# Performance work log

Measured on AMD Instinct MI355X. Metric: run time of the kernel, lower is better.

## Reference

```python
import jax, jax.numpy as jnp
import numpy as np

B, LX, LY = 64, 64, 64
E = 512          # enc_hid_size
D = 512          # dec_hid_size
NE = 512         # n_embed
H = 8            # n_head
E2 = 2 * E       # bidirectional annotation width


def setup_inputs() -> dict:
    key = jax.random.key(0)
    ks = iter(jax.random.split(key, 40))
    def rn(shape, scale=1.0):
        return jax.random.normal(next(ks), shape, dtype=jnp.float32) * scale
    s = lambda f: 1.0 / np.sqrt(f)
    return dict(
        xs_h=rn((B, LX, E2)),
        ys_e=rn((B, LY, NE)),
        xs_mask=jnp.ones((B, LX), jnp.float32),
        ys_mask=jnp.ones((B, LY), jnp.float32),
        W_sinit=rn((E2, D), s(E2)), b_sinit=jnp.zeros((D,), jnp.float32),
        W_keys=rn((E2, D), s(E2)),
        Wx_cell=rn((NE, 3 * D), s(NE)), bx_cell=jnp.zeros((3, D), jnp.float32), gx_cell=jnp.ones((3, D), jnp.float32),
        Wh_cell=rn((D, 3 * D), s(D)), gh_cell=jnp.ones((3, D), jnp.float32),
        Wx_cond=rn((E2, 3 * D), s(E2)), bx_cond=jnp.zeros((3, D), jnp.float32), gx_cond=jnp.ones((3, D), jnp.float32),
        Wh_cond=rn((D, 3 * D), s(D)), gh_cond=jnp.ones((3, D), jnp.float32),
        Wq=rn((D, D), s(D)), bq=jnp.zeros((D,), jnp.float32),
        V_att=rn((D, H), s(D)),
        Wo=rn((E2, E2), s(E2)), bo=jnp.zeros((E2,), jnp.float32),
        Wy=rn((NE, D), s(NE)), by=jnp.zeros((D,), jnp.float32),
        Wc=rn((E2, D), s(E2)), bc=jnp.zeros((D,), jnp.float32),
        Ws=rn((D, D), s(D)), bs=jnp.zeros((D,), jnp.float32),
    )


def _ln(v, eps=1e-5):
    mu = v.mean(-1, keepdims=True)
    var = ((v - mu) ** 2).mean(-1, keepdims=True)
    return (v - mu) * jax.lax.rsqrt(var + eps)


def _ln_gru(x, h, m, Wx, bx, gx, Wh, gh):
    # layer-normalized GRU transition cell (TransiLNCell), mask keeps old state on padding
    Bn = x.shape[0]
    ax = _ln((x @ Wx).reshape(Bn, 3, D)) * gx + bx   # (B,3,D), LN per gate chunk
    ah = _ln((h @ Wh).reshape(Bn, 3, D)) * gh
    r = jax.nn.sigmoid(ax[:, 0] + ah[:, 0])
    z = jax.nn.sigmoid(ax[:, 1] + ah[:, 1])
    hc = jnp.tanh(ax[:, 2] + r * ah[:, 2])
    hn = (1.0 - z) * h + z * hc
    return m[:, None] * hn + (1.0 - m[:, None]) * h


def _attend(s, xs_h, uh, xs_mask, Wq, bq, V, Wo, bo):
    # multihead additive attention: per-head additive scores, head-split values
    q = s @ Wq + bq                                   # (B,D)
    hid = jnp.tanh(uh + q[:, None, :])                # (B,L,D)
    e = jnp.einsum('bld,dh->blh', hid, V)             # (B,L,H)
    e = jnp.where(xs_mask[:, :, None] > 0, e, -1e9)
    alpha = jax.nn.softmax(e, axis=1)                 # (B,L,H)
    Bn, L, _ = xs_h.shape
    vals = xs_h.reshape(Bn, L, H, E2 // H)
    ctx = jnp.einsum('blh,blhv->bhv', alpha, vals).reshape(Bn, E2)
    return alpha, ctx @ Wo + bo


def reference(xs_h, ys_e, xs_mask, ys_mask,
              W_sinit, b_sinit, W_keys,
              Wx_cell, bx_cell, gx_cell, Wh_cell, gh_cell,
              Wx_cond, bx_cond, gx_cond, Wh_cond, gh_cond,
              Wq, bq, V_att, Wo, bo,
              Wy, by, Wc, bc, Ws, bs):
    # init_state: precompute attention keys, mean-pool annotations -> s0
    uh = xs_h @ W_keys                                          # (B,LX,D)
    pooled = (xs_h * xs_mask[:, :, None]).sum(1) / xs_mask.sum(1)[:, None]
    s0 = jnp.tanh(pooled @ W_sinit + b_sinit)                   # (B,D)

    def step(s_tm1, inp):
        y_tm1, ym = inp                                         # (B,NE), (B,)
        state = _ln_gru(y_tm1, s_tm1, ym, Wx_cell, bx_cell, gx_cell, Wh_cell, gh_cell)
        _, ctx = _attend(state, xs_h, uh, xs_mask, Wq, bq, V_att, Wo, bo)
        ctx = ctx * ym[:, None]
        s_t = _ln_gru(ctx, state, ym, Wx_cond, bx_cond, gx_cond, Wh_cond, gh_cond)
        # step_out: fused 3-way linear sum + tanh (max_out=False, dropout off in eval)
        logit = jnp.tanh(y_tm1 @ Wy + by + ctx @ Wc + bc + s_t @ Ws + bs)
        return s_t, logit

    ys_t = jnp.swapaxes(ys_e, 0, 1)      # (LY,B,NE) time-major
    ym_t = jnp.swapaxes(ys_mask, 0, 1)   # (LY,B)
    _, logits = jax.lax.scan(step, s0, (ys_t, ym_t))
    logits = jnp.swapaxes(logits, 0, 1)  # (B,LY,D)
    return logits * ys_mask[:, :, None]
```

## Files before the change

### kernel.cpp

```cpp
#include <hip/hip_runtime.h>
#include <math.h>

#define TPB 512
#define NWG 256

__device__ __forceinline__ float g_ld(const float* p){
    return __hip_atomic_load(p, __ATOMIC_RELAXED, __HIP_MEMORY_SCOPE_AGENT);
}
__device__ __forceinline__ void g_st(float* p, float v){
    __hip_atomic_store(p, v, __ATOMIC_RELAXED, __HIP_MEMORY_SCOPE_AGENT);
}
__device__ __forceinline__ float sigm(float x){ return 1.f/(1.f+expf(-x)); }

__global__ __launch_bounds__(TPB) void decoder_persistent(
    const float* __restrict__ xs_h, const float* __restrict__ ys_e,
    const float* __restrict__ xs_mask, const float* __restrict__ ys_mask,
    const float* __restrict__ W_sinit, const float* __restrict__ b_sinit,
    const float* __restrict__ W_keys,
    const float* __restrict__ Wx_cell, const float* __restrict__ bx_cell,
    const float* __restrict__ gx_cell, const float* __restrict__ Wh_cell,
    const float* __restrict__ gh_cell,
    const float* __restrict__ Wx_cond, const float* __restrict__ bx_cond,
    const float* __restrict__ gx_cond, const float* __restrict__ Wh_cond,
    const float* __restrict__ gh_cond,
    const float* __restrict__ Wq, const float* __restrict__ bq,
    const float* __restrict__ V_att, const float* __restrict__ Wo,
    const float* __restrict__ bo, const float* __restrict__ Wy,
    const float* __restrict__ by, const float* __restrict__ Wc,
    const float* __restrict__ bc, const float* __restrict__ Wsm,
    const float* __restrict__ bs,
    float* __restrict__ out, float* __restrict__ ws)
{
    const int w    = blockIdx.x;
    const int tid  = threadIdx.x;
    const int lane = tid & 63, wv = tid >> 6;
    const int i    = w & 7;
    const int grp  = w >> 3;
    const int b0   = grp * 2;

    unsigned* cntg = (unsigned*)ws + (size_t)grp * 16;
    float* AXn  = ws + 1024;
    float* uhP  = AXn  + (size_t)64*64*1536;
    float* YWbP = uhP  + (size_t)256*16*512;
    float* PB   = YWbP + (size_t)256*2*64*64;
    float* pb     = PB + (size_t)grp * 18432;
    float* tmpH_  = pb;
    float* tmpHC_ = pb + 3072;
    float* tmpXC_ = pb + 6144;
    float* qb_    = pb + 9216;
    float* e_     = pb + 10240;
    float* ctx0_  = pb + 11264;
    float* ctx_   = pb + 13312;
    float* pool_  = pb + 15360;
    float* s0_    = pb + 17408;

    __shared__ float sal[2][512];
    __shared__ float sbl[2][512];
    __shared__ float al[2][64];
    __shared__ float outcl[2][64];
    __shared__ float xml[2][64];
    __shared__ float red[8][24];
    __shared__ float red2[24];
    __shared__ float arena[13056];
    float* xv   = arena;
    float* comb = arena + 2048;

    unsigned gen = 0;
    auto gbar = [&](){
        __syncthreads();
        ++gen;
        if (tid == 0){
            __hip_atomic_fetch_add(cntg, 1u, __ATOMIC_RELAXED, __HIP_MEMORY_SCOPE_AGENT);
            while (__hip_atomic_load(cntg, __ATOMIC_RELAXED, __HIP_MEMORY_SCOPE_AGENT) < 8u*gen)
                __builtin_amdgcn_s_sleep(2);
        }
        asm volatile("" ::: "memory");
        __syncthreads();
    };

    auto breduce = [&](float* v, int nv){
        for (int n = 0; n < nv; ++n){
            float x = v[n];
            #pragma unroll
            for (int o = 32; o; o >>= 1) x += __shfl_xor(x, o);
            v[n] = x;
        }
        if (lane == 0) for (int n = 0; n < nv; ++n) red[wv][n] = v[n];
        __syncthreads();
        if (tid < nv){ float s = 0.f; for (int q = 0; q < 8; ++q) s += red[q][tid]; red2[tid] = s; }
        __syncthreads();
        for (int n = 0; n < nv; ++n) v[n] = red2[n];
    };

    auto gemv2 = [&](const float* Wa, int lda, int ca,
                     const float* Wb, int ldb, int cb, int CGA,
                     const float* x0, const float* x1, int K)->float{
        int cg = tid & 63, kq = tid >> 6;
        const float* W; int ld, col;
        if (cg < CGA){ W = Wa; ld = lda; col = ca + 4*cg; }
        else         { W = Wb; ld = ldb; col = cb + 4*(cg - CGA); }
        int Kq = K >> 3;
        const float* wp = W + (size_t)(kq*Kq)*ld + col;
        const float* xa = x0 + kq*Kq;
        const float* xb = x1 + kq*Kq;
        float a0=0,a1=0,a2=0,a3=0, c0=0,c1=0,c2=0,c3=0;
        for (int kk = 0; kk < Kq; kk += 8){
            float4 wr[8];
            #pragma unroll
            for (int u = 0; u < 8; ++u) wr[u] = *(const float4*)(wp + (size_t)(kk+u)*ld);
            #pragma unroll
            for (int u = 0; u < 8; ++u){
                float xA = xa[kk+u], xB = xb[kk+u];
                a0 = fmaf(xA, wr[u].x, a0); a1 = fmaf(xA, wr[u].y, a1);
                a2 = fmaf(xA, wr[u].z, a2); a3 = fmaf(xA, wr[u].w, a3);
                c0 = fmaf(xB, wr[u].x, c0); c1 = fmaf(xB, wr[u].y, c1);
                c2 = fmaf(xB, wr[u].z, c2); c3 = fmaf(xB, wr[u].w, c3);
            }
        }
        float* cp = comb + tid*9;
        cp[0]=a0; cp[1]=a1; cp[2]=a2; cp[3]=a3;
        cp[4]=c0; cp[5]=c1; cp[6]=c2; cp[7]=c3;
        __syncthreads();
        int bb = tid >> 8, c = tid & 255, cgq = c >> 2, j = c & 3;
        float s = 0.f;
        #pragma unroll
        for (int q = 0; q < 8; ++q) s += comb[(q*64 + cgq)*9 + bb*4 + j];
        __syncthreads();
        return s;
    };

    if (tid < 128) xml[tid>>6][tid&63] = xs_mask[(size_t)(b0 + (tid>>6))*64 + (tid&63)];
    __syncthreads();

    {
        int c4 = tid & 127, kq = tid >> 7;
        unsigned base[16];
        #pragma unroll
        for (int j = 0; j < 16; ++j){
            int bb = j >> 3, l = i*8 + (j & 7);
            base[j] = (unsigned)(((b0+bb)*64 + l)*1024 + kq*256);
        }
        const float* wp = W_keys + (size_t)(kq*256)*512 + 4*c4;
        float4 acc[16];
        #pragma unroll
        for (int j = 0; j < 16; ++j) acc[j] = make_float4(0.f,0.f,0.f,0.f);
        for (int kk = 0; kk < 256; ++kk){
            float4 wr = *(const float4*)(wp + (size_t)kk*512);
            #pragma unroll
            for (int j = 0; j < 16; ++j){
                float xr = xs_h[base[j] + kk];
                acc[j].x = fmaf(xr, wr.x, acc[j].x); acc[j].y = fmaf(xr, wr.y, acc[j].y);
                acc[j].z = fmaf(xr, wr.z, acc[j].z); acc[j].w = fmaf(xr, wr.w, acc[j].w);
            }
        }
        for (int r = 0; r < 16; ++r){
            float* cp = arena + tid*5;
            cp[0]=acc[r].x; cp[1]=acc[r].y; cp[2]=acc[r].z; cp[3]=acc[r].w;
            __syncthreads();
            int c = tid; float s = 0.f;
            #pragma unroll
            for (int q = 0; q < 4; ++q) s += arena[(q*128 + (c>>2))*5 + (c&3)];
            uhP[((size_t)w*16 + r)*512 + c] = s;
            __syncthreads();
        }
    }

    for (int g = 0; g < 3; ++g){
        int c4 = tid & 127, kq = tid >> 7;
        unsigned base[16];
        #pragma unroll
        for (int j = 0; j < 16; ++j){
            int bb = j >> 3, t = i*8 + (j & 7);
            base[j] = (unsigned)(((b0+bb)*64 + t)*512 + kq*128);
        }
        const float* wp = Wx_cell + (size_t)(kq*128)*1536 + g*512 + 4*c4;
        float4 acc[16];
        #pragma unroll
        for (int j = 0; j < 16; ++j) acc[j] = make_float4(0.f,0.f,0.f,0.f);
        for (int kk = 0; kk < 128; ++kk){
            float4 wr = *(const float4*)(wp + (size_t)kk*1536);
            #pragma unroll
            for (int j = 0; j < 16; ++j){
                float xr = ys_e[base[j] + kk];
                acc[j].x = fmaf(xr, wr.x, acc[j].x); acc[j].y = fmaf(xr, wr.y, acc[j].y);
                acc[j].z = fmaf(xr, wr.z, acc[j].z); acc[j].w = fmaf(xr, wr.w, acc[j].w);
            }
        }
        for (int r = 0; r < 16; ++r){
            float* cp = arena + tid*5;
            cp[0]=acc[r].x; cp[1]=acc[r].y; cp[2]=acc[r].z; cp[3]=acc[r].w;
            __syncthreads();
            int c = tid; float val = 0.f;
            #pragma unroll
            for (int q = 0; q < 4; ++q) val += arena[(q*128 + (c>>2))*5 + (c&3)];
            float s1[1] = { val };
            breduce(s1, 1);
            float mu = s1[0]*(1.f/512.f);
            float d = val - mu;
            float s2[1] = { d*d };
            breduce(s2, 1);
            float rstd = rsqrtf(s2[0]*(1.f/512.f) + 1e-5f);
            int bb = r >> 3, t = i*8 + (r & 7), cg2 = g*512 + c;
            g_st(&AXn[(((size_t)(b0+bb))*64 + t)*1536 + cg2],
                 d*rstd*gx_cell[cg2] + bx_cell[cg2]);
            __syncthreads();
        }
    }

    for (int cc = 0; cc < 8; ++cc){
        int c4 = tid & 15, kq = tid >> 4;
        unsigned base[16];
        #pragma unroll
        for (int r = 0; r < 16; ++r){
            int rg = cc*16 + r, bb = rg >> 6, t = rg & 63;
            base[r] = (unsigned)(((b0+bb)*64 + t)*512 + kq*16);
        }
        const float* wp = Wy + (size_t)(kq*16)*512 + i*64 + 4*c4;
        float4 acc[16];
        #pragma unroll
        for (int r = 0; r < 16; ++r) acc[r] = make_float4(0.f,0.f,0.f,0.f);
        for (int kk = 0; kk < 16; ++kk){
            float4 wr = *(const float4*)(wp + (size_t)kk*512);
            #pragma unroll
            for (int r = 0; r < 16; ++r){
                float xr = ys_e[base[r] + kk];
                acc[r].x = fmaf(xr, wr.x, acc[r].x); acc[r].y = fmaf(xr, wr.y, acc[r].y);
                acc[r].z = fmaf(xr, wr.z, acc[r].z); acc[r].w = fmaf(xr, wr.w, acc[r].w);
            }
        }
        for (int r = 0; r < 16; ++r){
            float* cp = arena + tid*5;
            cp[0]=acc[r].x; cp[1]=acc[r].y; cp[2]=acc[r].z; cp[3]=acc[r].w;
            __syncthreads();
            if (tid < 64){
                int c = tid; float s = 0.f;
                #pragma unroll
                for (int q = 0; q < 32; ++q) s += arena[(q*16 + (c>>2))*5 + (c&3)];
                int rg = cc*16 + r, bb = rg >> 6, t = rg & 63;
                YWbP[(((size_t)w*2 + bb)*64 + t)*64 + c] = s + by[i*64 + c];
            }
            __syncthreads();
        }
    }

    if (tid < 256){
        int bb = tid >> 7, c = i*128 + (tid & 127);
        float msum = 0.f;
        for (int l = 0; l < 64; ++l) msum += xml[bb][l];
        float a = 0.f;
        for (int l = 0; l < 64; ++l)
            a += xs_h[((size_t)(b0+bb)*64 + l)*1024 + c] * xml[bb][l];
        g_st(&pool_[bb*1024 + c], a / msum);
    }
    gbar();

    for (int k = tid; k < 2048; k += TPB) xv[k] = g_ld(&pool_[k]);
    __syncthreads();
    {
        int c4 = tid & 15, kq = tid >> 4;
        const float* wp = W_sinit + (size_t)(kq*32)*512 + i*64 + 4*c4;
        float4 A = make_float4(0.f,0.f,0.f,0.f), Bv = make_float4(0.f,0.f,0.f,0.f);
        for (int kk = 0; kk < 32; ++kk){
            float4 wr = *(const float4*)(wp + (size_t)kk*512);
            float xA = xv[kq*32 + kk], xB = xv[1024 + kq*32 + kk];
            A.x = fmaf(xA, wr.x, A.x); A.y = fmaf(xA, wr.y, A.y);
            A.z = fmaf(xA, wr.z, A.z); A.w = fmaf(xA, wr.w, A.w);
            Bv.x = fmaf(xB, wr.x, Bv.x); Bv.y = fmaf(xB, wr.y, Bv.y);
            Bv.z = fmaf(xB, wr.z, Bv.z); Bv.w = fmaf(xB, wr.w, Bv.w);
        }
        float* cp = comb + tid*9;
        cp[0]=A.x; cp[1]=A.y; cp[2]=A.z; cp[3]=A.w;
        cp[4]=Bv.x; cp[5]=Bv.y; cp[6]=Bv.z; cp[7]=Bv.w;
        __syncthreads();
        if (tid < 128){
            int bb = tid >> 6, c = tid & 63; float s = 0.f;
            #pragma unroll
            for (int q = 0; q < 32; ++q) s += comb[(q*16 + (c>>2))*9 + bb*4 + (c&3)];
            g_st(&s0_[bb*512 + i*64 + c], tanhf(s + b_sinit[i*64 + c]));
        }
        __syncthreads();
    }
    gbar();
    sal[0][tid] = g_ld(&s0_[tid]);
    sal[1][tid] = g_ld(&s0_[512 + tid]);
    __syncthreads();

    {
        float r0 = gemv2(Wsm, 512, i*64, Wh_cell, 1536, i*192, 16,
                         &sal[0][0], &sal[1][0], 512);
        int bb = tid >> 8, c = tid & 255;
        if (c >= 64) g_st(&tmpH_[bb*1536 + i*192 + (c - 64)], r0);
    }
    gbar();

    for (int t = 0; t < 64; ++t){
        float ymr[2] = { ys_mask[(size_t)b0*64 + t], ys_mask[(size_t)(b0+1)*64 + t] };

        {
            float th[2][3], ax[2][3], st[6];
            #pragma unroll
            for (int bb = 0; bb < 2; ++bb)
                #pragma unroll
                for (int g = 0; g < 3; ++g){
                    th[bb][g] = g_ld(&tmpH_[bb*1536 + g*512 + tid]);
                    ax[bb][g] = g_ld(&AXn[(((size_t)(b0+bb))*64 + t)*1536 + g*512 + tid]);
                    st[bb*3+g] = th[bb][g];
                }
            breduce(st, 6);
            float dv[2][3], st2[6];
            #pragma unroll
            for (int bb = 0; bb < 2; ++bb)
                #pragma unroll
                for (int g = 0; g < 3; ++g){
                    float mu = st[bb*3+g]*(1.f/512.f);
                    dv[bb][g] = th[bb][g] - mu;
                    st2[bb*3+g] = dv[bb][g]*dv[bb][g];
                }
            breduce(st2, 6);
            #pragma unroll
            for (int bb = 0; bb < 2; ++bb){
                float ah[3];
                #pragma unroll
                for (int g = 0; g < 3; ++g){
                    float var = st2[bb*3+g]*(1.f/512.f);
                    ah[g] = dv[bb][g]*rsqrtf(var + 1e-5f)*gh_cell[g*512 + tid];
                }
                float h  = sal[bb][tid];
                float r  = sigm(ax[bb][0] + ah[0]);
                float z  = sigm(ax[bb][1] + ah[1]);
                float hc = tanhf(ax[bb][2] + r*ah[2]);
                float hn = (1.f - z)*h + z*hc;
                sbl[bb][tid] = ymr[bb]*hn + (1.f - ymr[bb])*h;
            }
        }
        __syncthreads();
        {
            float ra = gemv2(Wq, 512, i*64, Wh_cond, 1536, i*192, 16,
                             &sbl[0][0], &sbl[1][0], 512);
            int bb = tid >> 8, c = tid & 255;
            if (c < 64){ int col = i*64 + c; g_st(&qb_[bb*512 + col], ra + bq[col]); }
            else g_st(&tmpHC_[bb*1536 + i*192 + (c - 64)], ra);
        }
        gbar();

        for (int k = tid; k < 1024; k += TPB) xv[k] = g_ld(&qb_[k]);
        __syncthreads();
        for (int jj = wv; jj < 16; jj += 8){
            int bb = jj >> 3, l = i*8 + (jj & 7);
            float acc[8] = {0.f,0.f,0.f,0.f,0.f,0.f,0.f,0.f};
            #pragma unroll
            for (int u = 0; u < 8; ++u){
                int d = u*64 + lane;
                float hid = tanhf(uhP[((size_t)w*16 + jj)*512 + d] + xv[bb*512 + d]);
                float4 va = *(const float4*)&V_att[(size_t)d*8];
                float4 vb = *(const float4*)&V_att[(size_t)d*8 + 4];
                acc[0] = fmaf(hid, va.x, acc[0]); acc[1] = fmaf(hid, va.y, acc[1]);
                acc[2] = fmaf(hid, va.z, acc[2]); acc[3] = fmaf(hid, va.w, acc[3]);
                acc[4] = fmaf(hid, vb.x, acc[4]); acc[5] = fmaf(hid, vb.y, acc[5]);
                acc[6] = fmaf(hid, vb.z, acc[6]); acc[7] = fmaf(hid, vb.w, acc[7]);
            }
            #pragma unroll
            for (int h = 0; h < 8; ++h)
                #pragma unroll
                for (int o = 32; o; o >>= 1) acc[h] += __shfl_xor(acc[h], o);
            if (lane == 0){
                float mk = xml[bb][l];
                #pragma unroll
                for (int h = 0; h < 8; ++h)
                    g_st(&e_[((size_t)bb*64 + l)*8 + h], (mk > 0.f) ? acc[h] : -1e9f);
            }
        }
        gbar();

        if (wv < 2){
            int bb = wv;
            float v = g_ld(&e_[((size_t)bb*64 + lane)*8 + i]);
            float mx = v;
            #pragma unroll
            for (int o = 32; o; o >>= 1) mx = fmaxf(mx, __shfl_xor(mx, o));
            float ex = expf(v - mx);
            float ss = ex;
            #pragma unroll
            for (int o = 32; o; o >>= 1) ss += __shfl_xor(ss, o);
            al[bb][lane] = ex / ss;
        }
        __syncthreads();
        {
            int kq = tid >> 6, job = tid & 63, bb = job >> 5, cg = job & 31;
            int c0 = i*128 + 4*cg;
            float4 a4 = make_float4(0.f,0.f,0.f,0.f);
            #pragma unroll
            for (int u = 0; u < 8; ++u){
                int l = kq*8 + u;
                float a = al[bb][l];
                float4 xw = *(const float4*)&xs_h[((size_t)(b0+bb)*64 + l)*1024 + c0];
                a4.x = fmaf(a, xw.x, a4.x); a4.y = fmaf(a, xw.y, a4.y);
                a4.z = fmaf(a, xw.z, a4.z); a4.w = fmaf(a, xw.w, a4.w);
            }
            float* cp = comb + tid*5;
            cp[0]=a4.x; cp[1]=a4.y; cp[2]=a4.z; cp[3]=a4.w;
            __syncthreads();
            if (tid < 256){
                int bb2 = tid >> 7, c = tid & 127; float s = 0.f;
                #pragma unroll
                for (int q = 0; q < 8; ++q) s += comb[(q*64 + bb2*32 + (c>>2))*5 + (c&3)];
                g_st(&ctx0_[bb2*1024 + i*128 + c], s);
            }
            __syncthreads();
        }
        gbar();

        for (int k = tid; k < 2048; k += TPB) xv[k] = g_ld(&ctx0_[k]);
        __syncthreads();
        {
            int kq = tid >> 5, cg = tid & 31;
            int c0 = i*128 + 4*cg;
            const float* wp = Wo + (size_t)(kq*64)*1024 + c0;
            const float* xa = xv + kq*64;
            const float* xb = xv + 1024 + kq*64;
            float a0=0,a1=0,a2=0,a3=0, d0=0,d1=0,d2=0,d3=0;
            for (int kk = 0; kk < 64; kk += 8){
                float4 wr[8];
                #pragma unroll
                for (int u = 0; u < 8; ++u) wr[u] = *(const float4*)(wp + (size_t)(kk+u)*1024);
                #pragma unroll
                for (int u = 0; u < 8; ++u){
                    float xA = xa[kk+u], xB = xb[kk+u];
                    a0 = fmaf(xA, wr[u].x, a0); a1 = fmaf(xA, wr[u].y, a1);
                    a2 = fmaf(xA, wr[u].z, a2); a3 = fmaf(xA, wr[u].w, a3);
                    d0 = fmaf(xB, wr[u].x, d0); d1 = fmaf(xB, wr[u].y, d1);
                    d2 = fmaf(xB, wr[u].z, d2); d3 = fmaf(xB, wr[u].w, d3);
                }
            }
            float* cp = comb + tid*9;
            cp[0]=a0; cp[1]=a1; cp[2]=a2; cp[3]=a3;
            cp[4]=d0; cp[5]=d1; cp[6]=d2; cp[7]=d3;
            __syncthreads();
            if (tid < 256){
                int bb2 = tid >> 7, c = tid & 127; float s = 0.f;
                #pragma unroll
                for (int q = 0; q < 16; ++q) s += comb[(q*32 + (c>>2))*9 + bb2*4 + (c&3)];
                float ym2 = bb2 ? ymr[1] : ymr[0];
                g_st(&ctx_[bb2*1024 + i*128 + c], (s + bo[i*128 + c]) * ym2);
            }
            __syncthreads();
        }
        gbar();

        for (int k = tid; k < 2048; k += TPB) xv[k] = g_ld(&ctx_[k]);
        __syncthreads();
        {
            float re = gemv2(Wx_cond, 1536, i*192, Wc, 512, i*64, 48,
                             &xv[0], &xv[1024], 1024);
            int bb = tid >> 8, c = tid & 255;
            if (c < 192){
                g_st(&tmpXC_[bb*1536 + i*192 + c], re);
            } else {
                outcl[bb][c - 192] = re;
            }
        }
        gbar();

        {
            float tx[2][3], th[2][3], st[12];
            #pragma unroll
            for (int bb = 0; bb < 2; ++bb)
                #pragma unroll
                for (int g = 0; g < 3; ++g){
                    tx[bb][g] = g_ld(&tmpXC_[bb*1536 + g*512 + tid]);
                    th[bb][g] = g_ld(&tmpHC_[bb*1536 + g*512 + tid]);
                    st[bb*3+g]     = tx[bb][g];
                    st[6 + bb*3+g] = th[bb][g];
                }
            breduce(st, 12);
            float dx[2][3], dh[2][3], st2[12];
            #pragma unroll
            for (int bb = 0; bb < 2; ++bb)
                #pragma unroll
                for (int g = 0; g < 3; ++g){
                    float mux = st[bb*3+g]*(1.f/512.f);
                    float muh = st[6 + bb*3+g]*(1.f/512.f);
                    dx[bb][g] = tx[bb][g] - mux;
                    dh[bb][g] = th[bb][g] - muh;
                    st2[bb*3+g]     = dx[bb][g]*dx[bb][g];
                    st2[6 + bb*3+g] = dh[bb][g]*dh[bb][g];
                }
            breduce(st2, 12);
            float snew[2];
            #pragma unroll
            for (int bb = 0; bb < 2; ++bb){
                float axc[3], ahc[3];
                #pragma unroll
                for (int g = 0; g < 3; ++g){
                    int c2 = g*512 + tid;
                    float vax = st2[bb*3+g]*(1.f/512.f);
                    float vah = st2[6 + bb*3+g]*(1.f/512.f);
                    axc[g] = dx[bb][g]*rsqrtf(vax + 1e-5f)*gx_cond[c2] + bx_cond[c2];
                    ahc[g] = dh[bb][g]*rsqrtf(vah + 1e-5f)*gh_cond[c2];
                }
                float h  = sbl[bb][tid];
                float r  = sigm(axc[0] + ahc[0]);
                float z  = sigm(axc[1] + ahc[1]);
                float hc = tanhf(axc[2] + r*ahc[2]);
                float hn = (1.f - z)*h + z*hc;
                snew[bb] = ymr[bb]*hn + (1.f - ymr[bb])*h;
            }
            sal[0][tid] = snew[0];
            sal[1][tid] = snew[1];
        }
        __syncthreads();
        {
            float rf = gemv2(Wsm, 512, i*64, Wh_cell, 1536, i*192, 16,
                             &sal[0][0], &sal[1][0], 512);
            int bb = tid >> 8, c = tid & 255;
            if (c < 64){
                int col = i*64 + c;
                float ymf = bb ? ymr[1] : ymr[0];
                float v = rf + YWbP[(((size_t)w*2 + bb)*64 + t)*64 + c]
                        + outcl[bb][c] + bc[col] + bs[col];
                out[(((size_t)(b0+bb))*64 + t)*512 + col] = tanhf(v)*ymf;
            } else {
                g_st(&tmpH_[bb*1536 + i*192 + (c - 64)], rf);
            }
        }
        gbar();
    }
}

extern "C" void kernel_launch(void* const* d_in, const int* in_sizes, int n_in,
                              void* d_out, int out_size, void* d_ws, size_t ws_size,
                              hipStream_t stream)
{
    hipMemsetAsync(d_ws, 0, 4096, stream);

    decoder_persistent<<<dim3(NWG), dim3(TPB), 0, stream>>>(
        (const float*)d_in[0],  (const float*)d_in[1],  (const float*)d_in[2],
        (const float*)d_in[3],  (const float*)d_in[4],  (const float*)d_in[5],
        (const float*)d_in[6],  (const float*)d_in[7],  (const float*)d_in[8],
        (const float*)d_in[9],  (const float*)d_in[10], (const float*)d_in[11],
        (const float*)d_in[12], (const float*)d_in[13], (const float*)d_in[14],
        (const float*)d_in[15], (const float*)d_in[16], (const float*)d_in[17],
        (const float*)d_in[18], (const float*)d_in[19], (const float*)d_in[20],
        (const float*)d_in[21], (const float*)d_in[22], (const float*)d_in[23],
        (const float*)d_in[24], (const float*)d_in[25], (const float*)d_in[26],
        (const float*)d_in[27],
        (float*)d_out, (float*)d_ws);
}
```

Measured before the change: 5.027 ms.

## Split work to one batch row per 8-workgroup group across 512 workgroups

Doubles the persistent grid from 256 to 512 workgroups so each group of 8 workgroups handles one batch row instead of two. Every gemv, LayerNorm and attention stage is rewritten for a single row, and shared memory and the workspace layout shrink to match. Launch bounds now request 4 blocks per SM so more of the grid fits at once. Each gemv now multiplies every weight by one vector instead of two, so weight traffic per useful FLOP doubles in exchange for more parallelism and shorter per-step work.

Measured after the change: 8.711 ms. +73.3%, slower.

```diff
diff --git a/kernel.cpp b/kernel.cpp
--- a/kernel.cpp
+++ b/kernel.cpp
@@ -2,7 +2,7 @@
 #include <math.h>
 
 #define TPB 512
-#define NWG 256
+#define NWG 512
 
 __device__ __forceinline__ float g_ld(const float* p){
     return __hip_atomic_load(p, __ATOMIC_RELAXED, __HIP_MEMORY_SCOPE_AGENT);
@@ -12,7 +12,7 @@
 }
 __device__ __forceinline__ float sigm(float x){ return 1.f/(1.f+expf(-x)); }
 
-__global__ __launch_bounds__(TPB) void decoder_persistent(
+__global__ __launch_bounds__(TPB, 4) void decoder_persistent(
     const float* __restrict__ xs_h, const float* __restrict__ ys_e,
     const float* __restrict__ xs_mask, const float* __restrict__ ys_mask,
     const float* __restrict__ W_sinit, const float* __restrict__ b_sinit,
@@ -36,34 +36,34 @@
     const int lane = tid & 63, wv = tid >> 6;
     const int i    = w & 7;
     const int grp  = w >> 3;
-    const int b0   = grp * 2;
+    const int b    = grp;
 
     unsigned* cntg = (unsigned*)ws + (size_t)grp * 16;
     float* AXn  = ws + 1024;
     float* uhP  = AXn  + (size_t)64*64*1536;
-    float* YWbP = uhP  + (size_t)256*16*512;
-    float* PB   = YWbP + (size_t)256*2*64*64;
-    float* pb     = PB + (size_t)grp * 18432;
+    float* YWbP = uhP  + (size_t)512*8*512;
+    float* PB   = YWbP + (size_t)512*64*64;
+    float* pb     = PB + (size_t)grp * 9216;
     float* tmpH_  = pb;
-    float* tmpHC_ = pb + 3072;
-    float* tmpXC_ = pb + 6144;
-    float* qb_    = pb + 9216;
-    float* e_     = pb + 10240;
-    float* ctx0_  = pb + 11264;
-    float* ctx_   = pb + 13312;
-    float* pool_  = pb + 15360;
-    float* s0_    = pb + 17408;
-
-    __shared__ float sal[2][512];
-    __shared__ float sbl[2][512];
-    __shared__ float al[2][64];
-    __shared__ float outcl[2][64];
-    __shared__ float xml[2][64];
-    __shared__ float red[8][24];
-    __shared__ float red2[24];
-    __shared__ float arena[13056];
+    float* tmpHC_ = pb + 1536;
+    float* tmpXC_ = pb + 3072;
+    float* qb_    = pb + 4608;
+    float* e_     = pb + 5120;
+    float* ctx0_  = pb + 5632;
+    float* ctx_   = pb + 6656;
+    float* pool_  = pb + 7680;
+    float* s0_    = pb + 8704;
+
+    __shared__ float sal[512];
+    __shared__ float sbl[512];
+    __shared__ float al[64];
+    __shared__ float outcl[64];
+    __shared__ float xml[64];
+    __shared__ float red[8][12];
+    __shared__ float red2[12];
+    __shared__ float arena[1024 + 2560];
     float* xv   = arena;
-    float* comb = arena + 2048;
+    float* comb = arena + 1024;
 
     unsigned gen = 0;
     auto gbar = [&](){
@@ -92,107 +92,101 @@
         for (int n = 0; n < nv; ++n) v[n] = red2[n];
     };
 
-    auto gemv2 = [&](const float* Wa, int lda, int ca,
+    auto gemv1 = [&](const float* Wa, int lda, int ca,
                      const float* Wb, int ldb, int cb, int CGA,
-                     const float* x0, const float* x1, int K)->float{
+                     const float* x, int K)->float{
         int cg = tid & 63, kq = tid >> 6;
         const float* W; int ld, col;
         if (cg < CGA){ W = Wa; ld = lda; col = ca + 4*cg; }
         else         { W = Wb; ld = ldb; col = cb + 4*(cg - CGA); }
         int Kq = K >> 3;
         const float* wp = W + (size_t)(kq*Kq)*ld + col;
-        const float* xa = x0 + kq*Kq;
-        const float* xb = x1 + kq*Kq;
-        float a0=0,a1=0,a2=0,a3=0, c0=0,c1=0,c2=0,c3=0;
+        const float* xa = x + kq*Kq;
+        float a0=0,a1=0,a2=0,a3=0;
         for (int kk = 0; kk < Kq; kk += 8){
             float4 wr[8];
             #pragma unroll
             for (int u = 0; u < 8; ++u) wr[u] = *(const float4*)(wp + (size_t)(kk+u)*ld);
             #pragma unroll
             for (int u = 0; u < 8; ++u){
-                float xA = xa[kk+u], xB = xb[kk+u];
+                float xA = xa[kk+u];
                 a0 = fmaf(xA, wr[u].x, a0); a1 = fmaf(xA, wr[u].y, a1);
                 a2 = fmaf(xA, wr[u].z, a2); a3 = fmaf(xA, wr[u].w, a3);
-                c0 = fmaf(xB, wr[u].x, c0); c1 = fmaf(xB, wr[u].y, c1);
-                c2 = fmaf(xB, wr[u].z, c2); c3 = fmaf(xB, wr[u].w, c3);
-            }
-        }
-        float* cp = comb + tid*9;
+            }
+        }
+        float* cp = comb + tid*5;
         cp[0]=a0; cp[1]=a1; cp[2]=a2; cp[3]=a3;
-        cp[4]=c0; cp[5]=c1; cp[6]=c2; cp[7]=c3;
-        __syncthreads();
-        int bb = tid >> 8, c = tid & 255, cgq = c >> 2, j = c & 3;
+        __syncthreads();
         float s = 0.f;
-        #pragma unroll
-        for (int q = 0; q < 8; ++q) s += comb[(q*64 + cgq)*9 + bb*4 + j];
+        if (tid < 256){
+            int c = tid, cgq = c >> 2, j = c & 3;
+            #pragma unroll
+            for (int q = 0; q < 8; ++q) s += comb[(q*64 + cgq)*5 + j];
+        }
         __syncthreads();
         return s;
     };
 
-    if (tid < 128) xml[tid>>6][tid&63] = xs_mask[(size_t)(b0 + (tid>>6))*64 + (tid&63)];
+    if (tid < 64) xml[tid] = xs_mask[(size_t)b*64 + tid];
     __syncthreads();
 
     {
         int c4 = tid & 127, kq = tid >> 7;
-        unsigned base[16];
+        unsigned base[8];
         #pragma unroll
-        for (int j = 0; j < 16; ++j){
-            int bb = j >> 3, l = i*8 + (j & 7);
-            base[j] = (unsigned)(((b0+bb)*64 + l)*1024 + kq*256);
-        }
+        for (int j = 0; j < 8; ++j)
+            base[j] = (unsigned)((b*64 + i*8 + j)*1024 + kq*256);
         const float* wp = W_keys + (size_t)(kq*256)*512 + 4*c4;
-        float4 acc[16];
+        float4 acc[8];
         #pragma unroll
-        for (int j = 0; j < 16; ++j) acc[j] = make_float4(0.f,0.f,0.f,0.f);
+        for (int j = 0; j < 8; ++j) acc[j] = make_float4(0.f,0.f,0.f,0.f);
         for (int kk = 0; kk < 256; ++kk){
             float4 wr = *(const float4*)(wp + (size_t)kk*512);
             #pragma unroll
-            for (int j = 0; j < 16; ++j){
+            for (int j = 0; j < 8; ++j){
                 float xr = xs_h[base[j] + kk];
                 acc[j].x = fmaf(xr, wr.x, acc[j].x); acc[j].y = fmaf(xr, wr.y, acc[j].y);
                 acc[j].z = fmaf(xr, wr.z, acc[j].z); acc[j].w = fmaf(xr, wr.w, acc[j].w);
             }
         }
-        for (int r = 0; r < 16; ++r){
-            float* cp = arena + tid*5;
+        for (int r = 0; r < 8; ++r){
+            float* cp = comb + tid*5;
             cp[0]=acc[r].x; cp[1]=acc[r].y; cp[2]=acc[r].z; cp[3]=acc[r].w;
             __syncthreads();
             int c = tid; float s = 0.f;
             #pragma unroll
-            for (int q = 0; q < 4; ++q) s += arena[(q*128 + (c>>2))*5 + (c&3)];
-            uhP[((size_t)w*16 + r)*512 + c] = s;
+            for (int q = 0; q < 4; ++q) s += comb[(q*128 + (c>>2))*5 + (c&3)];
+            uhP[((size_t)w*8 + r)*512 + c] = s;
             __syncthreads();
         }
     }
 
     for (int g = 0; g < 3; ++g){
         int c4 = tid & 127, kq = tid >> 7;
-        unsigned base[16];
+        unsigned base[8];
         #pragma unroll
-        for (int j = 0; j < 16; ++j){
-            int bb = j >> 3, t = i*8 + (j & 7);
-            base[j] = (unsigned)(((b0+bb)*64 + t)*512 + kq*128);
-        }
+        for (int j = 0; j < 8; ++j)
+            base[j] = (unsigned)((b*64 + i*8 + j)*512 + kq*128);
         const float* wp = Wx_cell + (size_t)(kq*128)*1536 + g*512 + 4*c4;
-        float4 acc[16];
+        float4 acc[8];
         #pragma unroll
-        for (int j = 0; j < 16; ++j) acc[j] = make_float4(0.f,0.f,0.f,0.f);
+        for (int j = 0; j < 8; ++j) acc[j] = make_float4(0.f,0.f,0.f,0.f);
         for (int kk = 0; kk < 128; ++kk){
             float4 wr = *(const float4*)(wp + (size_t)kk*1536);
             #pragma unroll
-            for (int j = 0; j < 16; ++j){
+            for (int j = 0; j < 8; ++j){
                 float xr = ys_e[base[j] + kk];
                 acc[j].x = fmaf(xr, wr.x, acc[j].x); acc[j].y = fmaf(xr, wr.y, acc[j].y);
                 acc[j].z = fmaf(xr, wr.z, acc[j].z); acc[j].w = fmaf(xr, wr.w, acc[j].w);
             }
         }
-        for (int r = 0; r < 16; ++r){
-            float* cp = arena + tid*5;
+        for (int r = 0; r < 8; ++r){
+            float* cp = comb + tid*5;
             cp[0]=acc[r].x; cp[1]=acc[r].y; cp[2]=acc[r].z; cp[3]=acc[r].w;
             __syncthreads();
             int c = tid; float val = 0.f;
             #pragma unroll
-            for (int q = 0; q < 4; ++q) val += arena[(q*128 + (c>>2))*5 + (c&3)];
+            for (int q = 0; q < 4; ++q) val += comb[(q*128 + (c>>2))*5 + (c&3)];
             float s1[1] = { val };
             breduce(s1, 1);
             float mu = s1[0]*(1.f/512.f);
@@ -200,21 +194,19 @@
             float s2[1] = { d*d };
             breduce(s2, 1);
             float rstd = rsqrtf(s2[0]*(1.f/512.f) + 1e-5f);
-            int bb = r >> 3, t = i*8 + (r & 7), cg2 = g*512 + c;
-            g_st(&AXn[(((size_t)(b0+bb))*64 + t)*1536 + cg2],
+            int t = i*8 + r, cg2 = g*512 + c;
+            g_st(&AXn[((size_t)b*64 + t)*1536 + cg2],
                  d*rstd*gx_cell[cg2] + bx_cell[cg2]);
             __syncthreads();
         }
     }
 
-    for (int cc = 0; cc < 8; ++cc){
+    for (int cc = 0; cc < 4; ++cc){
         int c4 = tid & 15, kq = tid >> 4;
         unsigned base[16];
         #pragma unroll
-        for (int r = 0; r < 16; ++r){
-            int rg = cc*16 + r, bb = rg >> 6, t = rg & 63;
-            base[r] = (unsigned)(((b0+bb)*64 + t)*512 + kq*16);
-        }
+        for (int r = 0; r < 16; ++r)
+            base[r] = (unsigned)((b*64 + cc*16 + r)*512 + kq*16);
         const float* wp = Wy + (size_t)(kq*16)*512 + i*64 + 4*c4;
         float4 acc[16];
         #pragma unroll
@@ -229,129 +221,117 @@
             }
         }
         for (int r = 0; r < 16; ++r){
-            float* cp = arena + tid*5;
+            float* cp = comb + tid*5;
             cp[0]=acc[r].x; cp[1]=acc[r].y; cp[2]=acc[r].z; cp[3]=acc[r].w;
             __syncthreads();
             if (tid < 64){
                 int c = tid; float s = 0.f;
                 #pragma unroll
-                for (int q = 0; q < 32; ++q) s += arena[(q*16 + (c>>2))*5 + (c&3)];
-                int rg = cc*16 + r, bb = rg >> 6, t = rg & 63;
-                YWbP[(((size_t)w*2 + bb)*64 + t)*64 + c] = s + by[i*64 + c];
-            }
-            __syncthreads();
-        }
-    }
-
-    if (tid < 256){
-        int bb = tid >> 7, c = i*128 + (tid & 127);
+                for (int q = 0; q < 32; ++q) s += comb[(q*16 + (c>>2))*5 + (c&3)];
+                YWbP[((size_t)w*64 + cc*16 + r)*64 + c] = s + by[i*64 + c];
+            }
+            __syncthreads();
+        }
+    }
+
+    if (tid < 128){
+        int c = i*128 + tid;
         float msum = 0.f;
-        for (int l = 0; l < 64; ++l) msum += xml[bb][l];
+        for (int l = 0; l < 64; ++l) msum += xml[l];
         float a = 0.f;
         for (int l = 0; l < 64; ++l)
-            a += xs_h[((size_t)(b0+bb)*64 + l)*1024 + c] * xml[bb][l];
-        g_st(&pool_[bb*1024 + c], a / msum);
+            a += xs_h[((size_t)b*64 + l)*1024 + c] * xml[l];
+        g_st(&pool_[c], a / msum);
     }
     gbar();
 
-    for (int k = tid; k < 2048; k += TPB) xv[k] = g_ld(&pool_[k]);
+    for (int k = tid; k < 1024; k += TPB) xv[k] = g_ld(&pool_[k]);
     __syncthreads();
     {
         int c4 = tid & 15, kq = tid >> 4;
         const float* wp = W_sinit + (size_t)(kq*32)*512 + i*64 + 4*c4;
-        float4 A = make_float4(0.f,0.f,0.f,0.f), Bv = make_float4(0.f,0.f,0.f,0.f);
+        float4 A = make_float4(0.f,0.f,0.f,0.f);
         for (int kk = 0; kk < 32; ++kk){
             float4 wr = *(const float4*)(wp + (size_t)kk*512);
-            float xA = xv[kq*32 + kk], xB = xv[1024 + kq*32 + kk];
+            float xA = xv[kq*32 + kk];
             A.x = fmaf(xA, wr.x, A.x); A.y = fmaf(xA, wr.y, A.y);
             A.z = fmaf(xA, wr.z, A.z); A.w = fmaf(xA, wr.w, A.w);
-            Bv.x = fmaf(xB, wr.x, Bv.x); Bv.y = fmaf(xB, wr.y, Bv.y);
-            Bv.z = fmaf(xB, wr.z, Bv.z); Bv.w = fmaf(xB, wr.w, Bv.w);
-        }
-        float* cp = comb + tid*9;
+        }
+        float* cp = comb + tid*5;
         cp[0]=A.x; cp[1]=A.y; cp[2]=A.z; cp[3]=A.w;
-        cp[4]=Bv.x; cp[5]=Bv.y; cp[6]=Bv.z; cp[7]=Bv.w;
-        __syncthreads();
-        if (tid < 128){
-            int bb = tid >> 6, c = tid & 63; float s = 0.f;
-            #pragma unroll
-            for (int q = 0; q < 32; ++q) s += comb[(q*16 + (c>>2))*9 + bb*4 + (c&3)];
-            g_st(&s0_[bb*512 + i*64 + c], tanhf(s + b_sinit[i*64 + c]));
+        __syncthreads();
+        if (tid < 64){
+            int c = tid; float s = 0.f;
+            #pragma unroll
+            for (int q = 0; q < 32; ++q) s += comb[(q*16 + (c>>2))*5 + (c&3)];
+            g_st(&s0_[i*64 + c], tanhf(s + b_sinit[i*64 + c]));
         }
         __syncthreads();
     }
     gbar();
-    sal[0][tid] = g_ld(&s0_[tid]);
-    sal[1][tid] = g_ld(&s0_[512 + tid]);
+    sal[tid] = g_ld(&s0_[tid]);
     __syncthreads();
 
     {
-        float r0 = gemv2(Wsm, 512, i*64, Wh_cell, 1536, i*192, 16,
-                         &sal[0][0], &sal[1][0], 512);
-        int bb = tid >> 8, c = tid & 255;
-        if (c >= 64) g_st(&tmpH_[bb*1536 + i*192 + (c - 64)], r0);
+        float r0 = gemv1(Wsm, 512, i*64, Wh_cell, 1536, i*192, 16, sal, 512);
+        if (tid < 256){
+            int c = tid;
+            if (c >= 64) g_st(&tmpH_[i*192 + (c - 64)], r0);
+        }
     }
     gbar();
 
     for (int t = 0; t < 64; ++t){
-        float ymr[2] = { ys_mask[(size_t)b0*64 + t], ys_mask[(size_t)(b0+1)*64 + t] };
-
-        {
-            float th[2][3], ax[2][3], st[6];
-            #pragma unroll
-            for (int bb = 0; bb < 2; ++bb)
-                #pragma unroll
-                for (int g = 0; g < 3; ++g){
-                    th[bb][g] = g_ld(&tmpH_[bb*1536 + g*512 + tid]);
-                    ax[bb][g] = g_ld(&AXn[(((size_t)(b0+bb))*64 + t)*1536 + g*512 + tid]);
-                    st[bb*3+g] = th[bb][g];
-                }
-            breduce(st, 6);
-            float dv[2][3], st2[6];
-            #pragma unroll
-            for (int bb = 0; bb < 2; ++bb)
-                #pragma unroll
-                for (int g = 0; g < 3; ++g){
-                    float mu = st[bb*3+g]*(1.f/512.f);
-                    dv[bb][g] = th[bb][g] - mu;
-                    st2[bb*3+g] = dv[bb][g]*dv[bb][g];
-                }
-            breduce(st2, 6);
-            #pragma unroll
-            for (int bb = 0; bb < 2; ++bb){
-                float ah[3];
-                #pragma unroll
-                for (int g = 0; g < 3; ++g){
-                    float var = st2[bb*3+g]*(1.f/512.f);
-                    ah[g] = dv[bb][g]*rsqrtf(var + 1e-5f)*gh_cell[g*512 + tid];
-                }
-                float h  = sal[bb][tid];
-                float r  = sigm(ax[bb][0] + ah[0]);
-                float z  = sigm(ax[bb][1] + ah[1]);
-                float hc = tanhf(ax[bb][2] + r*ah[2]);
-                float hn = (1.f - z)*h + z*hc;
-                sbl[bb][tid] = ymr[bb]*hn + (1.f - ymr[bb])*h;
-            }
-        }
-        __syncthreads();
-        {
-            float ra = gemv2(Wq, 512, i*64, Wh_cond, 1536, i*192, 16,
-                             &sbl[0][0], &sbl[1][0], 512);
-            int bb = tid >> 8, c = tid & 255;
-            if (c < 64){ int col = i*64 + c; g_st(&qb_[bb*512 + col], ra + bq[col]); }
-            else g_st(&tmpHC_[bb*1536 + i*192 + (c - 64)], ra);
+        const float ym = ys_mask[(size_t)b*64 + t];
+
+        {
+            float th[3], ax[3], st[3];
+            #pragma unroll
+            for (int g = 0; g < 3; ++g){
+                th[g] = g_ld(&tmpH_[g*512 + tid]);
+                ax[g] = g_ld(&AXn[((size_t)b*64 + t)*1536 + g*512 + tid]);
+                st[g] = th[g];
+            }
+            breduce(st, 3);
+            float dv[3], st2[3];
+            #pragma unroll
+            for (int g = 0; g < 3; ++g){
+                float mu = st[g]*(1.f/512.f);
+                dv[g] = th[g] - mu;
+                st2[g] = dv[g]*dv[g];
+            }
+            breduce(st2, 3);
+            float ah[3];
+            #pragma unroll
+            for (int g = 0; g < 3; ++g)
+                ah[g] = dv[g]*rsqrtf(st2[g]*(1.f/512.f) + 1e-5f)*gh_cell[g*512 + tid];
+            float h  = sal[tid];
+            float r  = sigm(ax[0] + ah[0]);
+            float z  = sigm(ax[1] + ah[1]);
+            float hc = tanhf(ax[2] + r*ah[2]);
+            float hn = (1.f - z)*h + z*hc;
+            sbl[tid] = ym*hn + (1.f - ym)*h;
+        }
+        __syncthreads();
+        {
+            float ra = gemv1(Wq, 512, i*64, Wh_cond, 1536, i*192, 16, sbl, 512);
+            if (tid < 256){
+                int c = tid;
+                if (c < 64){ int col = i*64 + c; g_st(&qb_[col], ra + bq[col]); }
+                else g_st(&tmpHC_[i*192 + (c - 64)], ra);
+            }
         }
         gbar();
 
-        for (int k = tid; k < 1024; k += TPB) xv[k] = g_ld(&qb_[k]);
-        __syncthreads();
-        for (int jj = wv; jj < 16; jj += 8){
-            int bb = jj >> 3, l = i*8 + (jj & 7);
+        xv[tid] = g_ld(&qb_[tid]);
+        __syncthreads();
+        {
+            int l = i*8 + wv;
             float acc[8] = {0.f,0.f,0.f,0.f,0.f,0.f,0.f,0.f};
             #pragma unroll
             for (int u = 0; u < 8; ++u){
                 int d = u*64 + lane;
-                float hid = tanhf(uhP[((size_t)w*16 + jj)*512 + d] + xv[bb*512 + d]);
+                float hid = tanhf(uhP[((size_t)w*8 + wv)*512 + d] + xv[d]);
                 float4 va = *(const float4*)&V_att[(size_t)d*8];
                 float4 vb = *(const float4*)&V_att[(size_t)d*8 + 4];
                 acc[0] = fmaf(hid, va.x, acc[0]); acc[1] = fmaf(hid, va.y, acc[1]);
@@ -364,17 +344,16 @@
                 #pragma unroll
                 for (int o = 32; o; o >>= 1) acc[h] += __shfl_xor(acc[h], o);
             if (lane == 0){
-                float mk = xml[bb][l];
+                float mk = xml[l];
                 #pragma unroll
                 for (int h = 0; h < 8; ++h)
-                    g_st(&e_[((size_t)bb*64 + l)*8 + h], (mk > 0.f) ? acc[h] : -1e9f);
+                    g_st(&e_[(size_t)l*8 + h], (mk > 0.f) ? acc[h] : -1e9f);
             }
         }
         gbar();
 
-        if (wv < 2){
-            int bb = wv;
-            float v = g_ld(&e_[((size_t)bb*64 + lane)*8 + i]);
+        if (wv == 0){
+            float v = g_ld(&e_[(size_t)lane*8 + i]);
             float mx = v;
             #pragma unroll
             for (int o = 32; o; o >>= 1) mx = fmaxf(mx, __shfl_xor(mx, o));
@@ -382,145 +361,128 @@
             float ss = ex;
             #pragma unroll
             for (int o = 32; o; o >>= 1) ss += __shfl_xor(ss, o);
-            al[bb][lane] = ex / ss;
-        }
-        __syncthreads();
-        {
-            int kq = tid >> 6, job = tid & 63, bb = job >> 5, cg = job & 31;
+            al[lane] = ex / ss;
+        }
+        __syncthreads();
+        {
+            int kq = tid >> 5, cg = tid & 31;
             int c0 = i*128 + 4*cg;
             float4 a4 = make_float4(0.f,0.f,0.f,0.f);
             #pragma unroll
-            for (int u = 0; u < 8; ++u){
-                int l = kq*8 + u;
-                float a = al[bb][l];
-                float4 xw = *(const float4*)&xs_h[((size_t)(b0+bb)*64 + l)*1024 + c0];
+            for (int u = 0; u < 4; ++u){
+                int l = kq*4 + u;
+                float a = al[l];
+                float4 xw = *(const float4*)&xs_h[((size_t)b*64 + l)*1024 + c0];
                 a4.x = fmaf(a, xw.x, a4.x); a4.y = fmaf(a, xw.y, a4.y);
                 a4.z = fmaf(a, xw.z, a4.z); a4.w = fmaf(a, xw.w, a4.w);
             }
             float* cp = comb + tid*5;
             cp[0]=a4.x; cp[1]=a4.y; cp[2]=a4.z; cp[3]=a4.w;
             __syncthreads();
-            if (tid < 256){
-                int bb2 = tid >> 7, c = tid & 127; float s = 0.f;
-                #pragma unroll
-                for (int q = 0; q < 8; ++q) s += comb[(q*64 + bb2*32 + (c>>2))*5 + (c&3)];
-                g_st(&ctx0_[bb2*1024 + i*128 + c], s);
+            if (tid < 128){
+                int c = tid; float s = 0.f;
+                #pragma unroll
+                for (int q = 0; q < 16; ++q) s += comb[(q*32 + (c>>2))*5 + (c&3)];
+                g_st(&ctx0_[i*128 + c], s);
             }
             __syncthreads();
         }
         gbar();
 
-        for (int k = tid; k < 2048; k += TPB) xv[k] = g_ld(&ctx0_[k]);
+        for (int k = tid; k < 1024; k += TPB) xv[k] = g_ld(&ctx0_[k]);
         __syncthreads();
         {
             int kq = tid >> 5, cg = tid & 31;
             int c0 = i*128 + 4*cg;
             const float* wp = Wo + (size_t)(kq*64)*1024 + c0;
             const float* xa = xv + kq*64;
-            const float* xb = xv + 1024 + kq*64;
-            float a0=0,a1=0,a2=0,a3=0, d0=0,d1=0,d2=0,d3=0;
+            float a0=0,a1=0,a2=0,a3=0;
             for (int kk = 0; kk < 64; kk += 8){
                 float4 wr[8];
                 #pragma unroll
                 for (int u = 0; u < 8; ++u) wr[u] = *(const float4*)(wp + (size_t)(kk+u)*1024);
                 #pragma unroll
                 for (int u = 0; u < 8; ++u){
-                    float xA = xa[kk+u], xB = xb[kk+u];
+                    float xA = xa[kk+u];
                     a0 = fmaf(xA, wr[u].x, a0); a1 = fmaf(xA, wr[u].y, a1);
                     a2 = fmaf(xA, wr[u].z, a2); a3 = fmaf(xA, wr[u].w, a3);
-                    d0 = fmaf(xB, wr[u].x, d0); d1 = fmaf(xB, wr[u].y, d1);
-                    d2 = fmaf(xB, wr[u].z, d2); d3 = fmaf(xB, wr[u].w, d3);
                 }
             }
-            float* cp = comb + tid*9;
+            float* cp = comb + tid*5;
             cp[0]=a0; cp[1]=a1; cp[2]=a2; cp[3]=a3;
-            cp[4]=d0; cp[5]=d1; cp[6]=d2; cp[7]=d3;
-            __syncthreads();
+            __syncthreads();
+            if (tid < 128){
+                int c = tid; float s = 0.f;
+                #pragma unroll
+                for (int q = 0; q < 16; ++q) s += comb[(q*32 + (c>>2))*5 + (c&3)];
+                g_st(&ctx_[i*128 + c], (s + bo[i*128 + c]) * ym);
+            }
+            __syncthreads();
+        }
+        gbar();
+
+        for (int k = tid; k < 1024; k += TPB) xv[k] = g_ld(&ctx_[k]);
+        __syncthreads();
+        {
+            float re = gemv1(Wx_cond, 1536, i*192, Wc, 512, i*64, 48, xv, 1024);
             if (tid < 256){
-                int bb2 = tid >> 7, c = tid & 127; float s = 0.f;
-                #pragma unroll
-                for (int q = 0; q < 16; ++q) s += comb[(q*32 + (c>>2))*9 + bb2*4 + (c&3)];
-                float ym2 = bb2 ? ymr[1] : ymr[0];
-                g_st(&ctx_[bb2*1024 + i*128 + c], (s + bo[i*128 + c]) * ym2);
-            }
-            __syncthreads();
+                int c = tid;
+                if (c < 192) g_st(&tmpXC_[i*192 + c], re);
+                else         outcl[c - 192] = re;
+            }
         }
         gbar();
 
-        for (int k = tid; k < 2048; k += TPB) xv[k] = g_ld(&ctx_[k]);
-        __syncthreads();
-        {
-            float re = gemv2(Wx_cond, 1536, i*192, Wc, 512, i*64, 48,
-                             &xv[0], &xv[1024], 1024);
-            int bb = tid >> 8, c = tid & 255;
-            if (c < 192){
-                g_st(&tmpXC_[bb*1536 + i*192 + c], re);
-            } else {
-                outcl[bb][c - 192] = re;
-            }
-        }
-        gbar();
-
-        {
-            float tx[2][3], th[2][3], st[12];
-            #pragma unroll
-            for (int bb = 0; bb < 2; ++bb)
-                #pragma unroll
-                for (int g = 0; g < 3; ++g){
-                    tx[bb][g] = g_ld(&tmpXC_[bb*1536 + g*512 + tid]);
-                    th[bb][g] = g_ld(&tmpHC_[bb*1536 + g*512 + tid]);
-                    st[bb*3+g]     = tx[bb][g];
-                    st[6 + bb*3+g] = th[bb][g];
+        {
+            float tx[3], th[3], st[6];
+            #pragma unroll
+            for (int g = 0; g < 3; ++g){
+                tx[g] = g_ld(&tmpXC_[g*512 + tid]);
+                th[g] = g_ld(&tmpHC_[g*512 + tid]);
+                st[g]     = tx[g];
+                st[3 + g] = th[g];
+            }
+            breduce(st, 6);
+            float dx[3], dh[3], st2[6];
+            #pragma unroll
+            for (int g = 0; g < 3; ++g){
+                float mux = st[g]*(1.f/512.f);
+                float muh = st[3 + g]*(1.f/512.f);
+                dx[g] = tx[g] - mux;
+                dh[g] = th[g] - muh;
+                st2[g]     = dx[g]*dx[g];
+                st2[3 + g] = dh[g]*dh[g];
+            }
+            breduce(st2, 6);
+            float axc[3], ahc[3];
+            #pragma unroll
+            for (int g = 0; g < 3; ++g){
+                int c2 = g*512 + tid;
+                axc[g] = dx[g]*rsqrtf(st2[g]*(1.f/512.f) + 1e-5f)*gx_cond[c2] + bx_cond[c2];
+                ahc[g] = dh[g]*rsqrtf(st2[3+g]*(1.f/512.f) + 1e-5f)*gh_cond[c2];
+            }
+            float h  = sbl[tid];
+            float r  = sigm(axc[0] + ahc[0]);
+            float z  = sigm(axc[1] + ahc[1]);
+            float hc = tanhf(axc[2] + r*ahc[2]);
+            float hn = (1.f - z)*h + z*hc;
+            float snew = ym*hn + (1.f - ym)*h;
+            __syncthreads();
+            sal[tid] = snew;
+        }
+        __syncthreads();
+        {
+            float rf = gemv1(Wsm, 512, i*64, Wh_cell, 1536, i*192, 16, sal, 512);
+            if (tid < 256){
+                int c = tid;
+                if (c < 64){
+                    int col = i*64 + c;
+                    float v = rf + YWbP[((size_t)w*64 + t)*64 + c]
+                            + outcl[c] + bc[col] + bs[col];
+                    out[((size_t)b*64 + t)*512 + col] = tanhf(v)*ym;
+                } else {
+                    g_st(&tmpH_[i*192 + (c - 64)], rf);
                 }
-            breduce(st, 12);
-            float dx[2][3], dh[2][3], st2[12];
-            #pragma unroll
-            for (int bb = 0; bb < 2; ++bb)
-                #pragma unroll
-                for (int g = 0; g < 3; ++g){
-                    float mux = st[bb*3+g]*(1.f/512.f);
-                    float muh = st[6 + bb*3+g]*(1.f/512.f);
-                    dx[bb][g] = tx[bb][g] - mux;
-                    dh[bb][g] = th[bb][g] - muh;
-                    st2[bb*3+g]     = dx[bb][g]*dx[bb][g];
-                    st2[6 + bb*3+g] = dh[bb][g]*dh[bb][g];
-                }
-            breduce(st2, 12);
-            float snew[2];
-            #pragma unroll
-            for (int bb = 0; bb < 2; ++bb){
-                float axc[3], ahc[3];
-                #pragma unroll
-                for (int g = 0; g < 3; ++g){
-                    int c2 = g*512 + tid;
-                    float vax = st2[bb*3+g]*(1.f/512.f);
-                    float vah = st2[6 + bb*3+g]*(1.f/512.f);
-                    axc[g] = dx[bb][g]*rsqrtf(vax + 1e-5f)*gx_cond[c2] + bx_cond[c2];
-                    ahc[g] = dh[bb][g]*rsqrtf(vah + 1e-5f)*gh_cond[c2];
-                }
-                float h  = sbl[bb][tid];
-                float r  = sigm(axc[0] + ahc[0]);
-                float z  = sigm(axc[1] + ahc[1]);
-                float hc = tanhf(axc[2] + r*ahc[2]);
-                float hn = (1.f - z)*h + z*hc;
-                snew[bb] = ymr[bb]*hn + (1.f - ymr[bb])*h;
-            }
-            sal[0][tid] = snew[0];
-            sal[1][tid] = snew[1];
-        }
-        __syncthreads();
-        {
-            float rf = gemv2(Wsm, 512, i*64, Wh_cell, 1536, i*192, 16,
-                             &sal[0][0], &sal[1][0], 512);
-            int bb = tid >> 8, c = tid & 255;
-            if (c < 64){
-                int col = i*64 + c;
-                float ymf = bb ? ymr[1] : ymr[0];
-                float v = rf + YWbP[(((size_t)w*2 + bb)*64 + t)*64 + c]
-                        + outcl[bb][c] + bc[col] + bs[col];
-                out[(((size_t)(b0+bb))*64 + t)*512 + col] = tanhf(v)*ymf;
-            } else {
-                g_st(&tmpH_[bb*1536 + i*192 + (c - 64)], rf);
             }
         }
         gbar();
```
